# Optimization experiments

Measured on AMD Instinct MI355X. Metric: run time of the kernel, lower is better.

## Reference

```python
import jax, jax.numpy as jnp
import numpy as np
import math

B, S, E, H = 2, 2048, 2048, 16
HD = E // H // 2  # 64, per-head dim of each differential half
DEPTH = 12
LAMBDA_INIT = 0.8 - 0.6 * math.exp(-0.3 * DEPTH)
EPS = 1e-5


def setup_inputs() -> dict:
    key = jax.random.key(0)
    ks = jax.random.split(key, 10)
    sc = 0.02
    return {
        "x": jax.random.normal(ks[0], (B, S, E), jnp.float32),
        "Wq": jax.random.normal(ks[1], (E, E), jnp.float32) * sc,
        "Wk": jax.random.normal(ks[2], (E, E), jnp.float32) * sc,
        "Wv": jax.random.normal(ks[3], (E, E), jnp.float32) * sc,
        "Wo": jax.random.normal(ks[4], (E, E), jnp.float32) * sc,
        "lambda_q1": jax.random.normal(ks[5], (HD,), jnp.float32) * 0.1,
        "lambda_k1": jax.random.normal(ks[6], (HD,), jnp.float32) * 0.1,
        "lambda_q2": jax.random.normal(ks[7], (HD,), jnp.float32) * 0.1,
        "lambda_k2": jax.random.normal(ks[8], (HD,), jnp.float32) * 0.1,
        "gamma": jnp.ones((2 * HD,), jnp.float32),
    }


def _rope_interleaved(x, cos, sin):
    # x: [b, s, h, d]; cos/sin: [s, d//2]; pairs are (0,1),(2,3),...
    xe, xo = x[..., 0::2], x[..., 1::2]
    c = cos[None, :, None, :]
    s = sin[None, :, None, :]
    oe = xe * c - xo * s
    oo = xe * s + xo * c
    return jnp.stack([oe, oo], axis=-1).reshape(x.shape)


def reference(x, Wq, Wk, Wv, Wo, lambda_q1, lambda_k1, lambda_q2, lambda_k2, gamma):
    b, t, _ = x.shape
    # rotary tables (rotary dim == HD, interleaved)
    angle = 1.0 / 10000 ** jnp.linspace(0.0, 1.0, HD // 2, dtype=jnp.float32)
    freqs = jnp.arange(t, dtype=jnp.float32)[:, None] * angle  # [t, HD//2]
    cos, sin = jnp.cos(freqs), jnp.sin(freqs)

    q = (x @ Wq.T).reshape(b, t, 2 * H, HD)
    k = (x @ Wk.T).reshape(b, t, 2 * H, HD)
    v = (x @ Wv.T).reshape(b, t, H, 2 * HD)  # concat(v1, v2) along last dim

    q = _rope_interleaved(q, cos, sin)
    k = _rope_interleaved(k, cos, sin)

    q = q.reshape(b, t, H, 2, HD)
    k = k.reshape(b, t, H, 2, HD)
    q1, q2 = q[:, :, :, 0], q[:, :, :, 1]
    k1, k2 = k[:, :, :, 0], k[:, :, :, 1]

    scale = HD ** -0.5  # flash_attn default softmax scale
    # branch 1: softmax(q1 k1) @ [v1|v2]
    s1 = jnp.einsum("bthd,bshd->bhts", q1, k1) * scale
    p1 = jax.nn.softmax(s1, axis=-1)
    o1 = jnp.einsum("bhts,bshd->bthd", p1, v)  # [b,t,H,2*HD]
    # branch 2: softmax(q2 k2) @ [v1|v2]
    s2 = jnp.einsum("bthd,bshd->bhts", q2, k2) * scale
    p2 = jax.nn.softmax(s2, axis=-1)
    o2 = jnp.einsum("bhts,bshd->bthd", p2, v)

    lam1 = jnp.exp(jnp.sum(lambda_q1 * lambda_k1))
    lam2 = jnp.exp(jnp.sum(lambda_q2 * lambda_k2))
    lam = lam1 - lam2 + LAMBDA_INIT

    attn = o1 - lam * o2  # [b,t,H,2*HD]
    # RMSNorm over last dim (2*HD) with affine gamma
    rms = jax.lax.rsqrt(jnp.mean(attn * attn, axis=-1, keepdims=True) + EPS)
    attn = attn * rms * gamma
    attn = attn * (1.0 - LAMBDA_INIT)
    attn = attn.reshape(b, t, H * 2 * HD)
    return attn @ Wo.T
```

## Files before the change

kernel.cpp:

```cpp
#include <hip/hip_runtime.h>
#include <cstdint>
#include <cstddef>

typedef unsigned short u16;
typedef __attribute__((ext_vector_type(8))) short short8;
typedef __attribute__((ext_vector_type(4))) float f32x4;
typedef __attribute__((ext_vector_type(16))) float f32x16;

#define MFMA_B16(a,b,c) __builtin_amdgcn_mfma_f32_16x16x32_bf16((a),(b),(c),0,0,0)
#define MFMA32(a,b,c)  __builtin_amdgcn_mfma_f32_32x32x16_bf16((a),(b),(c),0,0,0)

#define S_LEN 2048
#define EMB 2048
#define QKV_N 6144
#define HD 64
#define LAMBDA_INIT_F 0.78360576653162f
#define ONE_MINUS_LI 0.21639423346838f
#define EXP2_SCALE 0.18033688011112042f

static __device__ __forceinline__ u16 f2bf(float f) {
  unsigned u = __float_as_uint(f);
  unsigned r = ((u >> 16) & 1u) + 0x7fffu;
  return (u16)((u + r) >> 16);
}
static __device__ __forceinline__ float bf2f(u16 h) {
  return __uint_as_float(((unsigned)h) << 16);
}
static __device__ __forceinline__ unsigned cvt_pk_bf16(float lo, float hi) {
  unsigned r;
  asm("v_cvt_pk_bf16_f32 %0, %1, %2" : "=v"(r) : "v"(lo), "v"(hi));
  return r;
}
static __device__ __forceinline__ short8 ld64p(const char* base, int o0, int o1) {
  union { unsigned long long q[2]; short8 s; } x;
  x.q[0] = *(const unsigned long long*)(base + o0);
  x.q[1] = *(const unsigned long long*)(base + o1);
  return x.s;
}
static __device__ __forceinline__ void gload_lds16(const u16* g, u16* l) {
  __builtin_amdgcn_global_load_lds((const __attribute__((address_space(1))) void*)g,
                                   (__attribute__((address_space(3))) void*)l, 16, 0, 0);
}

__global__ void cvt_all(const float* __restrict__ x,  const float* __restrict__ Wq,
                        const float* __restrict__ Wk, const float* __restrict__ Wv,
                        const float* __restrict__ Wo,
                        u16* __restrict__ xb, u16* __restrict__ Wcat, u16* __restrict__ Wob) {
  const int NE = EMB * EMB;
  const int NE4 = NE / 4;
  int i = blockIdx.x * 256 + threadIdx.x;
  const float* s; u16* d; int j;
  if (i < 2 * NE4)      { s = x;  d = xb;            j = i;           }
  else if (i < 3 * NE4) { s = Wq; d = Wcat;          j = i - 2 * NE4; }
  else if (i < 4 * NE4) { s = Wk; d = Wcat + NE;     j = i - 3 * NE4; }
  else if (i < 5 * NE4) { s = Wv; d = Wcat + 2 * NE; j = i - 4 * NE4; }
  else                  { s = Wo; d = Wob;           j = i - 5 * NE4; }
  f32x4 v = *(const f32x4*)&s[j * 4];
  unsigned lo = cvt_pk_bf16(v[0], v[1]);
  unsigned hi = cvt_pk_bf16(v[2], v[3]);
  *(unsigned long long*)&d[j * 4] = (unsigned long long)lo | ((unsigned long long)hi << 32);
}

template <int BF16OUT>
__global__ __launch_bounds__(256, 2) void gemm_bt(const u16* __restrict__ A,
                                                  const u16* __restrict__ B,
                                                  void* __restrict__ Cout,
                                                  int M, int N, int K) {
  __shared__ u16 As[128 * 32];
  __shared__ u16 Bs[128 * 32];
  const int tid = threadIdx.x;
  const int lane = tid & 63, wv = tid >> 6;
  const int bm = blockIdx.x * 128, bn = blockIdx.y * 128;
  const int wr = (wv >> 1) * 64, wc = (wv & 1) * 64;
  const int lr = lane & 15, hk = lane >> 4;

  const int r0 = tid >> 2;
  const int c0 = (tid & 3) * 8;
  const u16* ga = A + (size_t)(bm + r0) * K + c0;
  const u16* gb = B + (size_t)(bn + r0) * K + c0;
  const size_t rstep = (size_t)64 * K;

  f32x4 acc[4][4] = {};

  for (int k0 = 0; k0 < K; k0 += 32) {
    __syncthreads();
    gload_lds16(ga + k0,         &As[(tid) * 8]);
    gload_lds16(ga + rstep + k0, &As[(tid + 256) * 8]);
    gload_lds16(gb + k0,         &Bs[(tid) * 8]);
    gload_lds16(gb + rstep + k0, &Bs[(tid + 256) * 8]);
    __syncthreads();
    short8 af[4], bfv[4];
#pragma unroll
    for (int i = 0; i < 4; i++) af[i] = *(const short8*)&As[(wr + i * 16 + lr) * 32 + hk * 8];
#pragma unroll
    for (int j = 0; j < 4; j++) bfv[j] = *(const short8*)&Bs[(wc + j * 16 + lr) * 32 + hk * 8];
#pragma unroll
    for (int i = 0; i < 4; i++)
#pragma unroll
      for (int j = 0; j < 4; j++)
        acc[i][j] = MFMA_B16(af[i], bfv[j], acc[i][j]);
  }

  if (BF16OUT) {
    u16* C = (u16*)Cout;
#pragma unroll
    for (int i = 0; i < 4; i++)
#pragma unroll
      for (int j = 0; j < 4; j++)
#pragma unroll
        for (int r = 0; r < 4; r++) {
          int row = bm + wr + i * 16 + hk * 4 + r;
          int col = bn + wc + j * 16 + lr;
          C[(size_t)row * N + col] = f2bf(acc[i][j][r]);
        }
  } else {
    float* C = (float*)Cout;
#pragma unroll
    for (int i = 0; i < 4; i++)
#pragma unroll
      for (int j = 0; j < 4; j++)
#pragma unroll
        for (int r = 0; r < 4; r++) {
          int row = bm + wr + i * 16 + hk * 4 + r;
          int col = bn + wc + j * 16 + lr;
          C[(size_t)row * N + col] = acc[i][j][r];
        }
  }
}

__global__ void rope_kernel(u16* __restrict__ qkv) {
  int idx = blockIdx.x * 256 + threadIdx.x;
  int p = idx & 31;
  int u = (idx >> 5) & 63;
  int m = idx >> 11;
  int t = m & (S_LEN - 1);
  int col = (u < 32) ? (u * 64 + 2 * p) : (EMB + (u - 32) * 64 + 2 * p);
  u16* ptr = qkv + (size_t)m * QKV_N + col;
  unsigned v = *(unsigned*)ptr;
  float xe = bf2f((u16)(v & 0xffff));
  float xo = bf2f((u16)(v >> 16));
  float w = expf((float)p * (-9.210340371976184f / 31.0f));
  float ang = (float)t * w;
  float sn, cs;
  sincosf(ang, &sn, &cs);
  float oe = xe * cs - xo * sn;
  float oo = xe * sn + xo * cs;
  *(unsigned*)ptr = (unsigned)f2bf(oe) | (((unsigned)f2bf(oo)) << 16);
}

#define SW(row, colByte)  ((((row)) << 7) + ((colByte) ^ (((row) & 7) << 4)))
#define SW8(row, colByte) ((((row)) << 7) + ((colByte) ^ (((row) & 15) << 3)))

__global__ __launch_bounds__(256, 2) void attn_kernel(
    const u16* __restrict__ qkv, u16* __restrict__ attnb,
    const float* __restrict__ lq1, const float* __restrict__ lk1,
    const float* __restrict__ lq2, const float* __restrict__ lk2,
    const float* __restrict__ gamma) {
  __shared__ u16 K1s[64 * 64];
  __shared__ u16 K2s[64 * 64];
  __shared__ u16 VTs[128 * 64];
  __shared__ u16 Ps[2 * 2 * 32 * 64];
  __shared__ float Lr[2][2][2][32];
  __shared__ float Sr[2][2][32];

  const int g = blockIdx.x;
  const int xcd = g & 7;
  const int gi = g >> 3;
  const int bh = xcd * 4 + (gi >> 5);
  const int qt = gi & 31;
  const int b = bh >> 4, h = bh & 15;

  const int tid = threadIdx.x, lane = tid & 63, wv = tid >> 6;
  const int qg = wv >> 1;
  const int dh = wv & 1;
  const int l31 = lane & 31;
  const int hi16 = (lane >> 5) * 16;
  const int hi8 = (lane >> 5) * 8;
  const int hi4 = (lane >> 5) * 4;

  float d1 = lq1[lane] * lk1[lane];
  float d2 = lq2[lane] * lk2[lane];
#pragma unroll
  for (int off = 32; off; off >>= 1) { d1 += __shfl_xor(d1, off); d2 += __shfl_xor(d2, off); }
  const float lam = __expf(d1) - __expf(d2) + LAMBDA_INIT_F;

  const int qbase = qt * 64 + qg * 32;
  const u16* qp1 = qkv + (size_t)(b * S_LEN + qbase + l31) * QKV_N + (2 * h) * 64;
  const u16* qp2 = qp1 + 64;
  short8 q1f0 = *(const short8*)(qp1 + hi8);
  short8 q1f1 = *(const short8*)(qp1 + 16 + hi8);
  short8 q1f2 = *(const short8*)(qp1 + 32 + hi8);
  short8 q1f3 = *(const short8*)(qp1 + 48 + hi8);
  short8 q2f0 = *(const short8*)(qp2 + hi8);
  short8 q2f1 = *(const short8*)(qp2 + 16 + hi8);
  short8 q2f2 = *(const short8*)(qp2 + 32 + hi8);
  short8 q2f3 = *(const short8*)(qp2 + 48 + hi8);

  f32x16 o1t0 = {}, o1t1 = {}, o2t0 = {}, o2t1 = {};
  float l1p = 0.f, l2p = 0.f;

  const int gl_row = wv * 8 + (lane >> 3);
  const int gl_cb  = ((lane & 7) ^ (lane >> 3)) * 8;
  u16* k1d = &K1s[(wv * 8) * 64 + lane * 8];
  u16* k2d = &K2s[(wv * 8) * 64 + lane * 8];

  const int vkv = (tid & 31) * 2;
  const int vd0 = (tid >> 5) * 8;

  const u16* kb1 = qkv + (size_t)b * S_LEN * QKV_N + EMB + (2 * h) * 64;
  const u16* kb2 = kb1 + 64;
  const u16* vbp = qkv + (size_t)b * S_LEN * QKV_N + 2 * EMB + h * 128;

  char* K1c = (char*)K1s;
  char* K2c = (char*)K2s;
  char* VTc = (char*)VTs;
  char* P1c = (char*)&Ps[(qg * 2 + 0) * 32 * 64];
  char* P2c = (char*)&Ps[(qg * 2 + 1) * 32 * 64];

  for (int kv0 = 0; kv0 < S_LEN; kv0 += 64) {
    __syncthreads();
    {
      const u16* g1 = kb1 + (size_t)(kv0 + gl_row) * QKV_N + gl_cb;
      const u16* g2 = kb2 + (size_t)(kv0 + gl_row) * QKV_N + gl_cb;
      gload_lds16(g1, k1d);
      gload_lds16(g1 + (size_t)32 * QKV_N, k1d + 32 * 64);
      gload_lds16(g2, k2d);
      gload_lds16(g2 + (size_t)32 * QKV_N, k2d + 32 * 64);
    }
    {
      const u16* vs = vbp + (size_t)(kv0 + vkv) * QKV_N + vd0;
      short8 a0 = *(const short8*)vs;
      short8 a1 = *(const short8*)(vs + QKV_N);
      short8 b0 = *(const short8*)(vs + 64);
      short8 b1 = *(const short8*)(vs + QKV_N + 64);
#pragma unroll
      for (int j = 0; j < 8; j++) {
        unsigned pk0 = (unsigned)(u16)a0[j] | (((unsigned)(u16)a1[j]) << 16);
        *(unsigned*)(VTc + SW8(vd0 + j, vkv * 2)) = pk0;
        unsigned pk1 = (unsigned)(u16)b0[j] | (((unsigned)(u16)b1[j]) << 16);
        *(unsigned*)(VTc + SW8(vd0 + 64 + j, vkv * 2)) = pk1;
      }
    }
    __syncthreads();

#define QKT(Kc, Q0, Q1, Q2, Q3, Pc, LSUM)                                        \
    do {                                                                         \
      f32x16 s = {};                                                             \
      int row = dh * 32 + l31;                                                   \
      s = MFMA32(*(const short8*)((Kc) + SW(row, 0  + hi16)), Q0, s);            \
      s = MFMA32(*(const short8*)((Kc) + SW(row, 32 + hi16)), Q1, s);            \
      s = MFMA32(*(const short8*)((Kc) + SW(row, 64 + hi16)), Q2, s);            \
      s = MFMA32(*(const short8*)((Kc) + SW(row, 96 + hi16)), Q3, s);            \
      _Pragma("unroll") for (int r = 0; r < 16; r += 4) {                        \
        float e0 = __builtin_amdgcn_exp2f(s[r]     * EXP2_SCALE);                \
        float e1 = __builtin_amdgcn_exp2f(s[r + 1] * EXP2_SCALE);                \
        float e2 = __builtin_amdgcn_exp2f(s[r + 2] * EXP2_SCALE);                \
        float e3 = __builtin_amdgcn_exp2f(s[r + 3] * EXP2_SCALE);                \
        LSUM += (e0 + e1) + (e2 + e3);                                           \
        unsigned lo_ = cvt_pk_bf16(e0, e1);                                      \
        unsigned hi_ = cvt_pk_bf16(e2, e3);                                      \
        *(unsigned long long*)((Pc) + SW8(l31, dh * 64 + (r >> 2) * 16 + hi8)) = \
            (unsigned long long)lo_ | ((unsigned long long)hi_ << 32);           \
      }                                                                          \
    } while (0)
    QKT(K1c, q1f0, q1f1, q1f2, q1f3, P1c, l1p);
    QKT(K2c, q2f0, q2f1, q2f2, q2f3, P2c, l2p);
#undef QKT
    __syncthreads();

    short8 p1f0 = ld64p(P1c, SW8(l31, 0  + hi16), SW8(l31, 8   + hi16));
    short8 p1f1 = ld64p(P1c, SW8(l31, 32 + hi16), SW8(l31, 40  + hi16));
    short8 p1f2 = ld64p(P1c, SW8(l31, 64 + hi16), SW8(l31, 72  + hi16));
    short8 p1f3 = ld64p(P1c, SW8(l31, 96 + hi16), SW8(l31, 104 + hi16));
    short8 p2f0 = ld64p(P2c, SW8(l31, 0  + hi16), SW8(l31, 8   + hi16));
    short8 p2f1 = ld64p(P2c, SW8(l31, 32 + hi16), SW8(l31, 40  + hi16));
    short8 p2f2 = ld64p(P2c, SW8(l31, 64 + hi16), SW8(l31, 72  + hi16));
    short8 p2f3 = ld64p(P2c, SW8(l31, 96 + hi16), SW8(l31, 104 + hi16));

#define PVD(DT, O1, O2)                                                          \
    do {                                                                         \
      int rw = (DT) * 32 + l31;                                                  \
      short8 va0 = ld64p(VTc, SW8(rw, 0  + hi16), SW8(rw, 8   + hi16));          \
      short8 va1 = ld64p(VTc, SW8(rw, 32 + hi16), SW8(rw, 40  + hi16));          \
      short8 va2 = ld64p(VTc, SW8(rw, 64 + hi16), SW8(rw, 72  + hi16));          \
      short8 va3 = ld64p(VTc, SW8(rw, 96 + hi16), SW8(rw, 104 + hi16));          \
      O1 = MFMA32(va0, p1f0, O1); O1 = MFMA32(va1, p1f1, O1);                    \
      O1 = MFMA32(va2, p1f2, O1); O1 = MFMA32(va3, p1f3, O1);                    \
      O2 = MFMA32(va0, p2f0, O2); O2 = MFMA32(va1, p2f1, O2);                    \
      O2 = MFMA32(va2, p2f2, O2); O2 = MFMA32(va3, p2f3, O2);                    \
    } while (0)
    PVD(dh * 2 + 0, o1t0, o2t0);
    PVD(dh * 2 + 1, o1t1, o2t1);
#undef PVD
  }

  float l1 = l1p + __shfl_xor(l1p, 32);
  float l2 = l2p + __shfl_xor(l2p, 32);
  if (lane < 32) { Lr[qg][0][dh][l31] = l1; Lr[qg][1][dh][l31] = l2; }
  __syncthreads();
  const float inv1 = 1.f / (Lr[qg][0][0][l31] + Lr[qg][0][1][l31]);
  const float inv2 = 1.f / (Lr[qg][1][0][l31] + Lr[qg][1][1][l31]);

  float ss = 0.f;
#define COMB(O1, O2)                                                   \
  _Pragma("unroll") for (int i = 0; i < 16; i++) {                     \
    float a = O1[i] * inv1 - lam * (O2[i] * inv2);                     \
    O1[i] = a;                                                         \
    ss += a * a;                                                       \
  }
  COMB(o1t0, o2t0) COMB(o1t1, o2t1)
#undef COMB
  ss += __shfl_xor(ss, 32);
  if (lane < 32) Sr[qg][dh][l31] = ss;
  __syncthreads();
  const float SS = Sr[qg][0][l31] + Sr[qg][1][l31];
  const float sc2 = rsqrtf(SS * (1.f / 128.f) + 1e-5f) * ONE_MINUS_LI;

  u16* orow = attnb + (size_t)(b * S_LEN + qbase + l31) * EMB + h * 128;
#define WRT(O1, DT)                                                             \
  _Pragma("unroll") for (int gg = 0; gg < 4; gg++) {                            \
    int d = dh * 64 + (DT) * 32 + gg * 8 + hi4;                                 \
    f32x4 gv = *(const f32x4*)&gamma[d];                                        \
    unsigned wlo = cvt_pk_bf16(O1[4 * gg] * gv[0] * sc2, O1[4 * gg + 1] * gv[1] * sc2); \
    unsigned whi = cvt_pk_bf16(O1[4 * gg + 2] * gv[2] * sc2, O1[4 * gg + 3] * gv[3] * sc2); \
    *(unsigned long long*)&orow[d] = (unsigned long long)wlo | ((unsigned long long)whi << 32); \
  }
  WRT(o1t0, 0) WRT(o1t1, 1)
#undef WRT
}

extern "C" void kernel_launch(void* const* d_in, const int* in_sizes, int n_in,
                              void* d_out, int out_size, void* d_ws, size_t ws_size,
                              hipStream_t stream) {
  (void)in_sizes; (void)n_in; (void)out_size; (void)ws_size;
  const float* x   = (const float*)d_in[0];
  const float* Wq  = (const float*)d_in[1];
  const float* Wk  = (const float*)d_in[2];
  const float* Wv  = (const float*)d_in[3];
  const float* Wo  = (const float*)d_in[4];
  const float* lq1 = (const float*)d_in[5];
  const float* lk1 = (const float*)d_in[6];
  const float* lq2 = (const float*)d_in[7];
  const float* lk2 = (const float*)d_in[8];
  const float* gam = (const float*)d_in[9];

  char* ws = (char*)d_ws;
  u16* xb    = (u16*)(ws);
  u16* Wcat  = (u16*)(ws + 16777216);
  u16* Wob   = (u16*)(ws + 41943040);
  u16* qkv   = (u16*)(ws + 50331648);
  u16* attnb = xb;

  const int NE = EMB * EMB;
  cvt_all<<<(6 * (NE / 4)) / 256, 256, 0, stream>>>(x, Wq, Wk, Wv, Wo, xb, Wcat, Wob);

  dim3 g1(4096 / 128, QKV_N / 128);
  gemm_bt<1><<<g1, 256, 0, stream>>>(xb, Wcat, qkv, 4096, QKV_N, EMB);

  rope_kernel<<<(4096 * 64 * 32) / 256, 256, 0, stream>>>(qkv);

  attn_kernel<<<1024, 256, 0, stream>>>(qkv, attnb, lq1, lk1, lq2, lk2, gam);

  dim3 g2(4096 / 128, EMB / 128);
  gemm_bt<0><<<g2, 256, 0, stream>>>(attnb, Wob, d_out, 4096, EMB, EMB);
}
```

Before: 360.2 us.

## Double-buffer GEMM with 128x256 tiles, BK=64, swizzled LDS, and simplify attention swizzle

Replaces the single-buffered 128x128, BK=32 GEMM with a 512-thread kernel that computes 128x256 tiles. It uses BK=64, XOR-swizzled LDS, and double-buffered global-to-LDS loads, so the loads for the next k-step overlap the MFMAs of the current one and one barrier per step is removed. The attention kernel's P and V^T LDS layout moves from an 8-byte swizzle with paired 64-bit loads to a 16-byte swizzle with single 128-bit loads. The cost is larger LDS use per block (96KB at launch bounds 2) and possible bank conflicts on the transposed V stores.

```diff
diff --git a/kernel.cpp b/kernel.cpp
--- a/kernel.cpp
+++ b/kernel.cpp
@@ -30,12 +30,6 @@
   unsigned r;
   asm("v_cvt_pk_bf16_f32 %0, %1, %2" : "=v"(r) : "v"(lo), "v"(hi));
   return r;
-}
-static __device__ __forceinline__ short8 ld64p(const char* base, int o0, int o1) {
-  union { unsigned long long q[2]; short8 s; } x;
-  x.q[0] = *(const unsigned long long*)(base + o0);
-  x.q[1] = *(const unsigned long long*)(base + o1);
-  return x.s;
 }
 static __device__ __forceinline__ void gload_lds16(const u16* g, u16* l) {
   __builtin_amdgcn_global_load_lds((const __attribute__((address_space(1))) void*)g,
@@ -61,45 +55,67 @@
   *(unsigned long long*)&d[j * 4] = (unsigned long long)lo | ((unsigned long long)hi << 32);
 }
 
+#define SWG(row, colByte) (((row) << 7) + ((colByte) ^ (((row) & 7) << 4)))
+
 template <int BF16OUT>
-__global__ __launch_bounds__(256, 2) void gemm_bt(const u16* __restrict__ A,
-                                                  const u16* __restrict__ B,
-                                                  void* __restrict__ Cout,
-                                                  int M, int N, int K) {
-  __shared__ u16 As[128 * 32];
-  __shared__ u16 Bs[128 * 32];
+__global__ __launch_bounds__(512, 2) void gemm2(const u16* __restrict__ A,
+                                                const u16* __restrict__ B,
+                                                void* __restrict__ Cout,
+                                                int M, int N, int K) {
+  __shared__ u16 As[2][128 * 64];
+  __shared__ u16 Bs[2][2][128 * 64];
   const int tid = threadIdx.x;
   const int lane = tid & 63, wv = tid >> 6;
-  const int bm = blockIdx.x * 128, bn = blockIdx.y * 128;
-  const int wr = (wv >> 1) * 64, wc = (wv & 1) * 64;
+  const int wr = wv >> 2, wc = wv & 3;
   const int lr = lane & 15, hk = lane >> 4;
-
-  const int r0 = tid >> 2;
-  const int c0 = (tid & 3) * 8;
-  const u16* ga = A + (size_t)(bm + r0) * K + c0;
-  const u16* gb = B + (size_t)(bn + r0) * K + c0;
-  const size_t rstep = (size_t)64 * K;
+  const int bm = blockIdx.x * 128, bn = blockIdx.y * 256;
+
+  const int srow = tid >> 3;
+  const int ssb  = tid & 7;
+  const int scb  = (ssb ^ (srow & 7)) * 8;
+  const u16* gA = A + (size_t)(bm + srow) * K + scb;
+  const u16* gB = B + (size_t)(bn + srow) * K + scb;
+  const int ldst = srow * 64 + ssb * 8;
 
   f32x4 acc[4][4] = {};
 
-  for (int k0 = 0; k0 < K; k0 += 32) {
+#define STAGE2(buf, k0_) do {                                              \
+    gload_lds16(gA + (k0_),                   &As[buf][ldst]);             \
+    gload_lds16(gA + (size_t)64  * K + (k0_), &As[buf][ldst + 64 * 64]);   \
+    gload_lds16(gB + (k0_),                   &Bs[buf][0][ldst]);          \
+    gload_lds16(gB + (size_t)64  * K + (k0_), &Bs[buf][0][ldst + 64 * 64]);\
+    gload_lds16(gB + (size_t)128 * K + (k0_), &Bs[buf][1][ldst]);          \
+    gload_lds16(gB + (size_t)192 * K + (k0_), &Bs[buf][1][ldst + 64 * 64]);\
+  } while (0)
+
+  STAGE2(0, 0);
+  __syncthreads();
+  int cur = 0;
+  const int br = (wc & 1) * 64;
+
+  for (int k0 = 0; k0 < K; k0 += 64) {
+    if (k0 + 64 < K) STAGE2(cur ^ 1, k0 + 64);
+    const char* aH = (const char*)&As[cur][0];
+    const char* bH = (const char*)&Bs[cur][wc >> 1][0];
+#pragma unroll
+    for (int kk = 0; kk < 2; kk++) {
+      short8 af[4], bfv[4];
+#pragma unroll
+      for (int i = 0; i < 4; i++)
+        af[i] = *(const short8*)(aH + SWG(wr * 64 + i * 16 + lr, kk * 64 + hk * 16));
+#pragma unroll
+      for (int j = 0; j < 4; j++)
+        bfv[j] = *(const short8*)(bH + SWG(br + j * 16 + lr, kk * 64 + hk * 16));
+#pragma unroll
+      for (int i = 0; i < 4; i++)
+#pragma unroll
+        for (int j = 0; j < 4; j++)
+          acc[i][j] = MFMA_B16(af[i], bfv[j], acc[i][j]);
+    }
     __syncthreads();
-    gload_lds16(ga + k0,         &As[(tid) * 8]);
-    gload_lds16(ga + rstep + k0, &As[(tid + 256) * 8]);
-    gload_lds16(gb + k0,         &Bs[(tid) * 8]);
-    gload_lds16(gb + rstep + k0, &Bs[(tid + 256) * 8]);
-    __syncthreads();
-    short8 af[4], bfv[4];
-#pragma unroll
-    for (int i = 0; i < 4; i++) af[i] = *(const short8*)&As[(wr + i * 16 + lr) * 32 + hk * 8];
-#pragma unroll
-    for (int j = 0; j < 4; j++) bfv[j] = *(const short8*)&Bs[(wc + j * 16 + lr) * 32 + hk * 8];
-#pragma unroll
-    for (int i = 0; i < 4; i++)
-#pragma unroll
-      for (int j = 0; j < 4; j++)
-        acc[i][j] = MFMA_B16(af[i], bfv[j], acc[i][j]);
-  }
+    cur ^= 1;
+  }
+#undef STAGE2
 
   if (BF16OUT) {
     u16* C = (u16*)Cout;
@@ -109,8 +125,8 @@
       for (int j = 0; j < 4; j++)
 #pragma unroll
         for (int r = 0; r < 4; r++) {
-          int row = bm + wr + i * 16 + hk * 4 + r;
-          int col = bn + wc + j * 16 + lr;
+          int row = bm + wr * 64 + i * 16 + hk * 4 + r;
+          int col = bn + wc * 64 + j * 16 + lr;
           C[(size_t)row * N + col] = f2bf(acc[i][j][r]);
         }
   } else {
@@ -121,8 +137,8 @@
       for (int j = 0; j < 4; j++)
 #pragma unroll
         for (int r = 0; r < 4; r++) {
-          int row = bm + wr + i * 16 + hk * 4 + r;
-          int col = bn + wc + j * 16 + lr;
+          int row = bm + wr * 64 + i * 16 + hk * 4 + r;
+          int col = bn + wc * 64 + j * 16 + lr;
           C[(size_t)row * N + col] = acc[i][j][r];
         }
   }
@@ -148,8 +164,7 @@
   *(unsigned*)ptr = (unsigned)f2bf(oe) | (((unsigned)f2bf(oo)) << 16);
 }
 
-#define SW(row, colByte)  ((((row)) << 7) + ((colByte) ^ (((row) & 7) << 4)))
-#define SW8(row, colByte) ((((row)) << 7) + ((colByte) ^ (((row) & 15) << 3)))
+#define SW(row, colByte) ((((row)) << 7) + ((colByte) ^ (((row) & 7) << 4)))
 
 __global__ __launch_bounds__(256, 2) void attn_kernel(
     const u16* __restrict__ qkv, u16* __restrict__ attnb,
@@ -236,9 +251,9 @@
 #pragma unroll
       for (int j = 0; j < 8; j++) {
         unsigned pk0 = (unsigned)(u16)a0[j] | (((unsigned)(u16)a1[j]) << 16);
-        *(unsigned*)(VTc + SW8(vd0 + j, vkv * 2)) = pk0;
+        *(unsigned*)(VTc + SW(vd0 + j, vkv * 2)) = pk0;
         unsigned pk1 = (unsigned)(u16)b0[j] | (((unsigned)(u16)b1[j]) << 16);
-        *(unsigned*)(VTc + SW8(vd0 + 64 + j, vkv * 2)) = pk1;
+        *(unsigned*)(VTc + SW(vd0 + 64 + j, vkv * 2)) = pk1;
       }
     }
     __syncthreads();
@@ -259,7 +274,7 @@
         LSUM += (e0 + e1) + (e2 + e3);                                           \
         unsigned lo_ = cvt_pk_bf16(e0, e1);                                      \
         unsigned hi_ = cvt_pk_bf16(e2, e3);                                      \
-        *(unsigned long long*)((Pc) + SW8(l31, dh * 64 + (r >> 2) * 16 + hi8)) = \
+        *(unsigned long long*)((Pc) + SW(l31, dh * 64 + (r >> 2) * 16 + hi8)) =  \
             (unsigned long long)lo_ | ((unsigned long long)hi_ << 32);           \
       }                                                                          \
     } while (0)
@@ -268,22 +283,22 @@
 #undef QKT
     __syncthreads();
 
-    short8 p1f0 = ld64p(P1c, SW8(l31, 0  + hi16), SW8(l31, 8   + hi16));
-    short8 p1f1 = ld64p(P1c, SW8(l31, 32 + hi16), SW8(l31, 40  + hi16));
-    short8 p1f2 = ld64p(P1c, SW8(l31, 64 + hi16), SW8(l31, 72  + hi16));
-    short8 p1f3 = ld64p(P1c, SW8(l31, 96 + hi16), SW8(l31, 104 + hi16));
-    short8 p2f0 = ld64p(P2c, SW8(l31, 0  + hi16), SW8(l31, 8   + hi16));
-    short8 p2f1 = ld64p(P2c, SW8(l31, 32 + hi16), SW8(l31, 40  + hi16));
-    short8 p2f2 = ld64p(P2c, SW8(l31, 64 + hi16), SW8(l31, 72  + hi16));
-    short8 p2f3 = ld64p(P2c, SW8(l31, 96 + hi16), SW8(l31, 104 + hi16));
+    short8 p1f0 = *(const short8*)(P1c + SW(l31, 0  + hi16));
+    short8 p1f1 = *(const short8*)(P1c + SW(l31, 32 + hi16));
+    short8 p1f2 = *(const short8*)(P1c + SW(l31, 64 + hi16));
+    short8 p1f3 = *(const short8*)(P1c + SW(l31, 96 + hi16));
+    short8 p2f0 = *(const short8*)(P2c + SW(l31, 0  + hi16));
+    short8 p2f1 = *(const short8*)(P2c + SW(l31, 32 + hi16));
+    short8 p2f2 = *(const short8*)(P2c + SW(l31, 64 + hi16));
+    short8 p2f3 = *(const short8*)(P2c + SW(l31, 96 + hi16));
 
 #define PVD(DT, O1, O2)                                                          \
     do {                                                                         \
       int rw = (DT) * 32 + l31;                                                  \
-      short8 va0 = ld64p(VTc, SW8(rw, 0  + hi16), SW8(rw, 8   + hi16));          \
-      short8 va1 = ld64p(VTc, SW8(rw, 32 + hi16), SW8(rw, 40  + hi16));          \
-      short8 va2 = ld64p(VTc, SW8(rw, 64 + hi16), SW8(rw, 72  + hi16));          \
-      short8 va3 = ld64p(VTc, SW8(rw, 96 + hi16), SW8(rw, 104 + hi16));          \
+      short8 va0 = *(const short8*)(VTc + SW(rw, 0  + hi16));                    \
+      short8 va1 = *(const short8*)(VTc + SW(rw, 32 + hi16));                    \
+      short8 va2 = *(const short8*)(VTc + SW(rw, 64 + hi16));                    \
+      short8 va3 = *(const short8*)(VTc + SW(rw, 96 + hi16));                    \
       O1 = MFMA32(va0, p1f0, O1); O1 = MFMA32(va1, p1f1, O1);                    \
       O1 = MFMA32(va2, p1f2, O1); O1 = MFMA32(va3, p1f3, O1);                    \
       O2 = MFMA32(va0, p2f0, O2); O2 = MFMA32(va1, p2f1, O2);                    \
@@ -354,13 +369,13 @@
   const int NE = EMB * EMB;
   cvt_all<<<(6 * (NE / 4)) / 256, 256, 0, stream>>>(x, Wq, Wk, Wv, Wo, xb, Wcat, Wob);
 
-  dim3 g1(4096 / 128, QKV_N / 128);
-  gemm_bt<1><<<g1, 256, 0, stream>>>(xb, Wcat, qkv, 4096, QKV_N, EMB);
+  dim3 g1(4096 / 128, QKV_N / 256);
+  gemm2<1><<<g1, 512, 0, stream>>>(xb, Wcat, qkv, 4096, QKV_N, EMB);
 
   rope_kernel<<<(4096 * 64 * 32) / 256, 256, 0, stream>>>(qkv);
 
   attn_kernel<<<1024, 256, 0, stream>>>(qkv, attnb, lq1, lk1, lq2, lk2, gam);
 
-  dim3 g2(4096 / 128, EMB / 128);
-  gemm_bt<0><<<g2, 256, 0, stream>>>(attnb, Wob, d_out, 4096, EMB, EMB);
-}
+  dim3 g2(4096 / 128, EMB / 256);
+  gemm2<0><<<g2, 512, 0, stream>>>(attnb, Wob, d_out, 4096, EMB, EMB);
+}
```

New measurement: 355.8 us. About the same (-1.2%).
